# Performance work log

Measured on AMD Instinct MI355X. Metric: run time of the kernel, lower is better.

## Reference

```python
import jax, jax.numpy as jnp
import numpy as np

EPS = 1e-12  # torch F.normalize clamp_min eps
NUM_HEADS = 4


def setup_inputs() -> dict:
    key = jax.random.key(0)
    ks = jax.random.split(key, 6)
    B, N, C = 8, 8192, 256
    x1 = jax.random.normal(ks[0], (B, N, C), dtype=jnp.float32)
    x2 = jax.random.normal(ks[1], (B, N, C), dtype=jnp.float32)
    s = 1.0 / np.sqrt(C)
    Wq = jax.random.normal(ks[2], (C, C), dtype=jnp.float32) * s
    Wk = jax.random.normal(ks[3], (C, C), dtype=jnp.float32) * s
    Wv = jax.random.normal(ks[4], (C, C), dtype=jnp.float32) * s
    Wo = jax.random.normal(ks[5], (C, C), dtype=jnp.float32) * s
    bo = jnp.zeros((C,), dtype=jnp.float32)
    temperature = jnp.ones((NUM_HEADS, 1, 1), dtype=jnp.float32)
    return {"x1": x1, "x2": x2, "Wq": Wq, "Wk": Wk, "Wv": Wv,
            "Wo": Wo, "bo": bo, "temperature": temperature}


def reference(x1, x2, Wq, Wk, Wv, Wo, bo, temperature):
    B, N, C = x1.shape
    H = NUM_HEADS
    d = C // H
    # Linear projections (torch Linear: y = x W^T), then [B,H,d,N] layout
    q = (x1 @ Wq.T).reshape(B, N, H, d).transpose(0, 2, 3, 1)  # [B,H,d,N]
    k = (x2 @ Wk.T).reshape(B, N, H, d).transpose(0, 2, 3, 1)  # [B,H,d,N]
    v = (x2 @ Wv.T).reshape(B, N, H, d).transpose(0, 2, 3, 1)  # [B,H,d,N]
    # L2-normalize along the token axis (dim=-1)
    qn = q / jnp.maximum(jnp.linalg.norm(q, axis=-1, keepdims=True), EPS)
    kn = k / jnp.maximum(jnp.linalg.norm(k, axis=-1, keepdims=True), EPS)
    # Channel-wise cross-covariance attention: [B,H,d,d]
    attn = jnp.einsum('bhdn,bhen->bhde', qn, kn) * temperature
    attn = jax.nn.softmax(attn, axis=-1)
    # (dropout is identity in eval mode)
    x_cross = jnp.einsum('bhde,bhen->bhdn', attn, v)  # [B,H,d,N]
    x_cross = x_cross.transpose(0, 3, 1, 2).reshape(B, N, C)  # [B,N,C]
    return x_cross @ Wo.T + bo
```

## Files before the change

### kernel.cpp

```cpp
#include <hip/hip_runtime.h>
#include <hip/hip_bf16.h>

#define BDIM 8
#define NTOK 8192
#define CDIM 256
#define HEADS 4
#define DHEAD 64
#define MROWS (BDIM * NTOK)
#define NSLAB 16

typedef unsigned short ushort_t;
typedef short bf16x8 __attribute__((ext_vector_type(8)));
typedef float f32x4 __attribute__((ext_vector_type(4)));
typedef unsigned short u16x8 __attribute__((ext_vector_type(8)));
typedef unsigned short u16x4 __attribute__((ext_vector_type(4)));

__device__ inline ushort_t f2bf(float f) {
    __hip_bfloat16 h = __float2bfloat16(f);
    return *reinterpret_cast<ushort_t*>(&h);
}

__device__ inline u16x8 pack8(float4 a, float4 b) {
    u16x8 o;
    o[0] = f2bf(a.x); o[1] = f2bf(a.y); o[2] = f2bf(a.z); o[3] = f2bf(a.w);
    o[4] = f2bf(b.x); o[5] = f2bf(b.y); o[6] = f2bf(b.z); o[7] = f2bf(b.w);
    return o;
}

__global__ __launch_bounds__(256) void zero_kernel(float* __restrict__ p, int n) {
    int i = blockIdx.x * 256 + threadIdx.x;
    if (i < n) p[i] = 0.0f;
}

__global__ __launch_bounds__(256) void proj_mfma(
    const float* __restrict__ x1, const float* __restrict__ x2,
    const float* __restrict__ Wq, const float* __restrict__ Wk,
    const float* __restrict__ Wv,
    ushort_t* __restrict__ qp, ushort_t* __restrict__ kp, ushort_t* __restrict__ vp,
    float* __restrict__ ssq, float* __restrict__ ssk)
{
    const float* A; const float* W; ushort_t* outp; float* ss;
    if (blockIdx.z == 0)      { A = x1; W = Wq; outp = qp; ss = ssq; }
    else if (blockIdx.z == 1) { A = x2; W = Wk; outp = kp; ss = ssk; }
    else                      { A = x2; W = Wv; outp = vp; ss = nullptr; }

    __shared__ ushort_t Asl[2][4096];
    __shared__ ushort_t Bsl[2][4096];
    __shared__ float colss[128];

    const int t = threadIdx.x;
    const int lane = t & 63, w = t >> 6;
    const int l16 = lane & 15, quad = lane >> 4;
    const int m0 = blockIdx.x * 128, c0 = blockIdx.y * 128;
    const int wm = (w >> 1) * 64, wn = (w & 1) * 64;

    const int srow = t >> 1;
    const int skh  = t & 1;

    const float* Ap = A + (size_t)(m0 + srow) * CDIM + skh * 16;
    const float* Wp = W + (size_t)(c0 + srow) * CDIM + skh * 16;

    float4 ga[4], gb[4];
#pragma unroll
    for (int i = 0; i < 4; ++i) {
        ga[i] = *(const float4*)(Ap + i * 4);
        gb[i] = *(const float4*)(Wp + i * 4);
    }

    f32x4 acc[4][4] = {};

#pragma unroll 2
    for (int it = 0; it < 8; ++it) {
        ushort_t* As = Asl[it & 1];
        ushort_t* Bs = Bsl[it & 1];
        *(u16x8*)&As[(skh * 2 + 0) * 1024 + srow * 8] = pack8(ga[0], ga[1]);
        *(u16x8*)&As[(skh * 2 + 1) * 1024 + srow * 8] = pack8(ga[2], ga[3]);
        *(u16x8*)&Bs[(skh * 2 + 0) * 1024 + srow * 8] = pack8(gb[0], gb[1]);
        *(u16x8*)&Bs[(skh * 2 + 1) * 1024 + srow * 8] = pack8(gb[2], gb[3]);
        if (it < 7) {
            int ko = (it + 1) * 32;
#pragma unroll
            for (int i = 0; i < 4; ++i) {
                ga[i] = *(const float4*)(Ap + ko + i * 4);
                gb[i] = *(const float4*)(Wp + ko + i * 4);
            }
        }
        asm volatile("s_waitcnt lgkmcnt(0)" ::: "memory");
        __builtin_amdgcn_s_barrier();
        bf16x8 aF[4], bF[4];
#pragma unroll
        for (int i = 0; i < 4; ++i)
            aF[i] = *(const bf16x8*)&As[quad * 1024 + (wm + i * 16 + l16) * 8];
#pragma unroll
        for (int j = 0; j < 4; ++j)
            bF[j] = *(const bf16x8*)&Bs[quad * 1024 + (wn + j * 16 + l16) * 8];
#pragma unroll
        for (int i = 0; i < 4; ++i)
#pragma unroll
            for (int j = 0; j < 4; ++j)
                acc[i][j] = __builtin_amdgcn_mfma_f32_16x16x32_bf16(aF[i], bF[j], acc[i][j], 0, 0, 0);
    }

#pragma unroll
    for (int i = 0; i < 4; ++i) {
#pragma unroll
        for (int j = 0; j < 4; ++j) {
            int col = c0 + wn + j * 16 + l16;
#pragma unroll
            for (int reg = 0; reg < 4; ++reg) {
                int row = m0 + wm + i * 16 + quad * 4 + reg;
                outp[(size_t)row * CDIM + col] = f2bf(acc[i][j][reg]);
            }
        }
    }

    if (ss) {
        __syncthreads();
        if (t < 128) colss[t] = 0.0f;
        __syncthreads();
#pragma unroll
        for (int j = 0; j < 4; ++j) {
            float s = 0.0f;
#pragma unroll
            for (int i = 0; i < 4; ++i)
#pragma unroll
                for (int reg = 0; reg < 4; ++reg)
                    s += acc[i][j][reg] * acc[i][j][reg];
            atomicAdd(&colss[wn + j * 16 + l16], s);
        }
        __syncthreads();
        if (t < 128) {
            int b = m0 >> 13;
            atomicAdd(&ss[b * CDIM + c0 + t], colss[t]);
        }
    }
}

__global__ __launch_bounds__(256) void gram_mfma(
    const ushort_t* __restrict__ qp, const ushort_t* __restrict__ kp,
    float* __restrict__ Gpart)
{
    constexpr int NS = 144;
    __shared__ ushort_t qs[64 * NS];
    __shared__ ushort_t ks2[64 * NS];
    __shared__ float gsum[4096];

    const int t = threadIdx.x;
    const int lane = t & 63, w = t >> 6;
    const int l16 = lane & 15, quad = lane >> 4;
    const int slab = blockIdx.x, h = blockIdx.y, b = blockIdx.z;
    const size_t base = (size_t)b * NTOK * CDIM + h * DHEAD;

    const int cg  = t >> 5;
    const int ng4 = t & 31;

    for (int i = t; i < 4096; i += 256) gsum[i] = 0.0f;

    f32x4 acc[4][4] = {};

    u16x8 qv[2][4], kv[2][4];
#pragma unroll
    for (int i = 0; i < 4; ++i) {
        size_t g = base + (size_t)(slab * 512 + ng4 * 4 + i) * CDIM + cg * 8;
        qv[0][i] = *(const u16x8*)&qp[g];
        kv[0][i] = *(const u16x8*)&kp[g];
    }

#pragma unroll
    for (int cch = 0; cch < 4; ++cch) {
        const int p = cch & 1;
        __syncthreads();
#pragma unroll
        for (int j = 0; j < 8; ++j) {
            u16x4 wq, wk;
            wq[0] = qv[p][0][j]; wq[1] = qv[p][1][j]; wq[2] = qv[p][2][j]; wq[3] = qv[p][3][j];
            wk[0] = kv[p][0][j]; wk[1] = kv[p][1][j]; wk[2] = kv[p][2][j]; wk[3] = kv[p][3][j];
            *(u16x4*)&qs[(cg * 8 + j) * NS + ng4 * 4] = wq;
            *(u16x4*)&ks2[(cg * 8 + j) * NS + ng4 * 4] = wk;
        }
        if (cch < 3) {
#pragma unroll
            for (int i = 0; i < 4; ++i) {
                size_t g = base + (size_t)(slab * 512 + (cch + 1) * 128 + ng4 * 4 + i) * CDIM + cg * 8;
                qv[p ^ 1][i] = *(const u16x8*)&qp[g];
                kv[p ^ 1][i] = *(const u16x8*)&kp[g];
            }
        }
        __syncthreads();
        bf16x8 aF[4], bF[4];
#pragma unroll
        for (int i = 0; i < 4; ++i)
            aF[i] = *(const bf16x8*)&qs[(i * 16 + l16) * NS + w * 32 + quad * 8];
#pragma unroll
        for (int j = 0; j < 4; ++j)
            bF[j] = *(const bf16x8*)&ks2[(j * 16 + l16) * NS + w * 32 + quad * 8];
#pragma unroll
        for (int i = 0; i < 4; ++i)
#pragma unroll
            for (int j = 0; j < 4; ++j)
                acc[i][j] = __builtin_amdgcn_mfma_f32_16x16x32_bf16(aF[i], bF[j], acc[i][j], 0, 0, 0);
    }

    __syncthreads();
#pragma unroll
    for (int i = 0; i < 4; ++i)
#pragma unroll
        for (int j = 0; j < 4; ++j)
#pragma unroll
            for (int reg = 0; reg < 4; ++reg)
                atomicAdd(&gsum[(i * 16 + quad * 4 + reg) * 64 + j * 16 + l16], acc[i][j][reg]);
    __syncthreads();

    float* Gp = Gpart + ((size_t)slab * BDIM * HEADS + b * HEADS + h) * 4096;
    for (int i = t; i < 4096; i += 256) Gp[i] = gsum[i];
}

__global__ __launch_bounds__(256) void softmax_weff(
    const float* __restrict__ Gpart, const float* __restrict__ ssq,
    const float* __restrict__ ssk, const float* __restrict__ temp,
    const float* __restrict__ Wo, ushort_t* __restrict__ Weffb)
{
    const int h = blockIdx.x, b = blockIdx.y;
    const int t = threadIdx.x;
    __shared__ float at[64][65];
    __shared__ float nk[64];

    if (t < 64) nk[t] = fmaxf(sqrtf(ssk[b * CDIM + h * DHEAD + t]), 1e-12f);
    __syncthreads();

    {
        const int row = t >> 2, part = t & 3;
        const size_t sstride = (size_t)BDIM * HEADS * 4096;
        const float* Gbase = Gpart + (size_t)(b * HEADS + h) * 4096 + row * 64 + part * 16;
        const float tmp = temp[h];
        const float nq = fmaxf(sqrtf(ssq[b * CDIM + h * DHEAD + row]), 1e-12f);

        float sum[16];
#pragma unroll
        for (int j = 0; j < 16; ++j) sum[j] = 0.0f;
#pragma unroll
        for (int s = 0; s < NSLAB; ++s) {
            const float4* gp = (const float4*)(Gbase + (size_t)s * sstride);
#pragma unroll
            for (int q4 = 0; q4 < 4; ++q4) {
                float4 v = gp[q4];
                sum[q4 * 4 + 0] += v.x; sum[q4 * 4 + 1] += v.y;
                sum[q4 * 4 + 2] += v.z; sum[q4 * 4 + 3] += v.w;
            }
        }

        float vals[16];
        float mx = -1e30f;
#pragma unroll
        for (int j = 0; j < 16; ++j) {
            int e = part * 16 + j;
            float v = sum[j] / (nq * nk[e]) * tmp;
            vals[j] = v;
            mx = fmaxf(mx, v);
        }
        mx = fmaxf(mx, __shfl_xor(mx, 1));
        mx = fmaxf(mx, __shfl_xor(mx, 2));
        float s = 0.0f;
#pragma unroll
        for (int j = 0; j < 16; ++j) {
            float ev = __expf(vals[j] - mx);
            vals[j] = ev;
            s += ev;
        }
        s += __shfl_xor(s, 1);
        s += __shfl_xor(s, 2);
        float inv = 1.0f / s;
#pragma unroll
        for (int j = 0; j < 16; ++j)
            at[row][part * 16 + j] = vals[j] * inv;
    }
    __syncthreads();

    const int c = t;
    float wo[64];
#pragma unroll
    for (int d2 = 0; d2 < 64; ++d2) wo[d2] = Wo[(size_t)c * CDIM + h * DHEAD + d2];

    ushort_t* Wb = Weffb + (size_t)b * CDIM * CDIM + (size_t)c * CDIM + h * DHEAD;
#pragma unroll 4
    for (int e = 0; e < 64; ++e) {
        float s = 0.0f;
#pragma unroll
        for (int d2 = 0; d2 < 64; ++d2) s += wo[d2] * at[d2][e];
        Wb[e] = f2bf(s);
    }
}

__global__ __launch_bounds__(256) void out_mfma(
    const ushort_t* __restrict__ vp, const ushort_t* __restrict__ Weffb,
    const float* __restrict__ bo, float* __restrict__ out)
{
    __shared__ ushort_t Asl[2][4096];
    __shared__ ushort_t Bsl[2][4096];

    const int t = threadIdx.x;
    const int lane = t & 63, w = t >> 6;
    const int l16 = lane & 15, quad = lane >> 4;
    const int m0 = blockIdx.x * 128, c0 = blockIdx.y * 128;
    const int wm = (w >> 1) * 64, wn = (w & 1) * 64;

    const int srow = t >> 1;
    const int skh  = t & 1;

    const ushort_t* Ap = vp + (size_t)(m0 + srow) * CDIM + skh * 16;
    const ushort_t* Bp = Weffb + (size_t)(m0 >> 13) * CDIM * CDIM
                       + (size_t)(c0 + srow) * CDIM + skh * 16;

    u16x8 ga0 = *(const u16x8*)Ap,       ga1 = *(const u16x8*)(Ap + 8);
    u16x8 gb0 = *(const u16x8*)Bp,       gb1 = *(const u16x8*)(Bp + 8);

    f32x4 acc[4][4] = {};

#pragma unroll 2
    for (int it = 0; it < 8; ++it) {
        ushort_t* As = Asl[it & 1];
        ushort_t* Bs = Bsl[it & 1];
        *(u16x8*)&As[(skh * 2 + 0) * 1024 + srow * 8] = ga0;
        *(u16x8*)&As[(skh * 2 + 1) * 1024 + srow * 8] = ga1;
        *(u16x8*)&Bs[(skh * 2 + 0) * 1024 + srow * 8] = gb0;
        *(u16x8*)&Bs[(skh * 2 + 1) * 1024 + srow * 8] = gb1;
        if (it < 7) {
            int ko = (it + 1) * 32;
            ga0 = *(const u16x8*)(Ap + ko);
            ga1 = *(const u16x8*)(Ap + ko + 8);
            gb0 = *(const u16x8*)(Bp + ko);
            gb1 = *(const u16x8*)(Bp + ko + 8);
        }
        asm volatile("s_waitcnt lgkmcnt(0)" ::: "memory");
        __builtin_amdgcn_s_barrier();
        bf16x8 aF[4], bF[4];
#pragma unroll
        for (int i = 0; i < 4; ++i)
            aF[i] = *(const bf16x8*)&As[quad * 1024 + (wm + i * 16 + l16) * 8];
#pragma unroll
        for (int j = 0; j < 4; ++j)
            bF[j] = *(const bf16x8*)&Bs[quad * 1024 + (wn + j * 16 + l16) * 8];
#pragma unroll
        for (int i = 0; i < 4; ++i)
#pragma unroll
            for (int j = 0; j < 4; ++j)
                acc[i][j] = __builtin_amdgcn_mfma_f32_16x16x32_bf16(aF[i], bF[j], acc[i][j], 0, 0, 0);
    }

#pragma unroll
    for (int i = 0; i < 4; ++i) {
#pragma unroll
        for (int j = 0; j < 4; ++j) {
            int col = c0 + wn + j * 16 + l16;
            float bias = bo[col];
#pragma unroll
            for (int reg = 0; reg < 4; ++reg) {
                int row = m0 + wm + i * 16 + quad * 4 + reg;
                out[(size_t)row * CDIM + col] = acc[i][j][reg] + bias;
            }
        }
    }
}

extern "C" void kernel_launch(void* const* d_in, const int* in_sizes, int n_in,
                              void* d_out, int out_size, void* d_ws, size_t ws_size,
                              hipStream_t stream) {
    const float* x1   = (const float*)d_in[0];
    const float* x2   = (const float*)d_in[1];
    const float* Wq   = (const float*)d_in[2];
    const float* Wk   = (const float*)d_in[3];
    const float* Wv   = (const float*)d_in[4];
    const float* Wo   = (const float*)d_in[5];
    const float* bo   = (const float*)d_in[6];
    const float* temp = (const float*)d_in[7];
    float* out = (float*)d_out;

    char* ws = (char*)d_ws;
    const size_t SZP = (size_t)MROWS * CDIM * sizeof(ushort_t);
    ushort_t* qp   = (ushort_t*)(ws);
    ushort_t* kp   = (ushort_t*)(ws + SZP);
    ushort_t* vp   = (ushort_t*)(ws + 2 * SZP);
    float*    ssq  = (float*)(ws + 3 * SZP);
    float*    ssk  = (float*)(ws + 3 * SZP + 8192);
    float*    Gpart= (float*)(ws + 3 * SZP + 16384);
    ushort_t* Weffb= (ushort_t*)(ws + 3 * SZP + 16384 + (size_t)NSLAB * BDIM * HEADS * 4096 * 4);

    zero_kernel<<<dim3((4096 + 255) / 256), dim3(256), 0, stream>>>(ssq, 4096);

    proj_mfma<<<dim3(MROWS / 128, CDIM / 128, 3), dim3(256), 0, stream>>>(
        x1, x2, Wq, Wk, Wv, qp, kp, vp, ssq, ssk);

    gram_mfma<<<dim3(NSLAB, HEADS, BDIM), dim3(256), 0, stream>>>(qp, kp, Gpart);

    softmax_weff<<<dim3(HEADS, BDIM), dim3(256), 0, stream>>>(Gpart, ssq, ssk, temp, Wo, Weffb);

    out_mfma<<<dim3(MROWS / 128, CDIM / 128), dim3(256), 0, stream>>>(vp, Weffb, bo, out);
}
```

Before: 351.6 us.

## Stream projection and output GEMMs without LDS using pre-converted bf16 weights

Adds a prep kernel that converts Wq/Wk/Wv to bf16 once and zeroes the sum-of-squares buffers, which replaces the zero kernel. The projection and output GEMMs are rewritten so each block covers 64 rows by all 256 columns. A rows feed straight into MFMA fragments from registers, and weight fragments are read directly from global memory, relying on L2 for reuse. This removes the LDS staging, barriers, and the repeated re-reading and re-conversion of A across column tiles. Column sums of squares use shuffles and one atomic per column per block. The risk is heavy reliance on uncoalesced global weight loads and higher register pressure.

```diff
diff --git a/kernel.cpp b/kernel.cpp
--- a/kernel.cpp
+++ b/kernel.cpp
@@ -27,112 +27,93 @@
     return o;
 }
 
-__global__ __launch_bounds__(256) void zero_kernel(float* __restrict__ p, int n) {
-    int i = blockIdx.x * 256 + threadIdx.x;
-    if (i < n) p[i] = 0.0f;
-}
-
-__global__ __launch_bounds__(256) void proj_mfma(
+__device__ inline bf16x8 as_bf(u16x8 v) { return *(bf16x8*)&v; }
+
+__global__ __launch_bounds__(256) void prep_kernel(
+    const float* __restrict__ Wq, const float* __restrict__ Wk,
+    const float* __restrict__ Wv, ushort_t* __restrict__ wb,
+    float* __restrict__ ss)
+{
+    const int bid = blockIdx.x;
+    if (bid < 96) {
+        int idx = (bid * 256 + threadIdx.x) * 8;
+        const float* src = (idx < 65536) ? Wq : (idx < 131072) ? Wk : Wv;
+        int off = idx & 65535;
+        float4 a = *(const float4*)(src + off);
+        float4 b = *(const float4*)(src + off + 4);
+        *(u16x8*)(wb + idx) = pack8(a, b);
+    } else {
+        int i = (bid - 96) * 256 + threadIdx.x;
+        if (i < 4096) ss[i] = 0.0f;
+    }
+}
+
+__global__ __launch_bounds__(256) void proj_stream(
     const float* __restrict__ x1, const float* __restrict__ x2,
-    const float* __restrict__ Wq, const float* __restrict__ Wk,
-    const float* __restrict__ Wv,
+    const ushort_t* __restrict__ wb,
     ushort_t* __restrict__ qp, ushort_t* __restrict__ kp, ushort_t* __restrict__ vp,
     float* __restrict__ ssq, float* __restrict__ ssk)
 {
-    const float* A; const float* W; ushort_t* outp; float* ss;
-    if (blockIdx.z == 0)      { A = x1; W = Wq; outp = qp; ss = ssq; }
-    else if (blockIdx.z == 1) { A = x2; W = Wk; outp = kp; ss = ssk; }
-    else                      { A = x2; W = Wv; outp = vp; ss = nullptr; }
-
-    __shared__ ushort_t Asl[2][4096];
-    __shared__ ushort_t Bsl[2][4096];
-    __shared__ float colss[128];
+    __shared__ float colw[4][256];
+
+    const float* A; const ushort_t* W; ushort_t* outp; float* ss;
+    if (blockIdx.y == 0)      { A = x1; W = wb;          outp = qp; ss = ssq; }
+    else if (blockIdx.y == 1) { A = x2; W = wb + 65536;  outp = kp; ss = ssk; }
+    else                      { A = x2; W = wb + 131072; outp = vp; ss = nullptr; }
 
     const int t = threadIdx.x;
     const int lane = t & 63, w = t >> 6;
     const int l16 = lane & 15, quad = lane >> 4;
-    const int m0 = blockIdx.x * 128, c0 = blockIdx.y * 128;
-    const int wm = (w >> 1) * 64, wn = (w & 1) * 64;
-
-    const int srow = t >> 1;
-    const int skh  = t & 1;
-
-    const float* Ap = A + (size_t)(m0 + srow) * CDIM + skh * 16;
-    const float* Wp = W + (size_t)(c0 + srow) * CDIM + skh * 16;
-
-    float4 ga[4], gb[4];
-#pragma unroll
-    for (int i = 0; i < 4; ++i) {
-        ga[i] = *(const float4*)(Ap + i * 4);
-        gb[i] = *(const float4*)(Wp + i * 4);
-    }
-
-    f32x4 acc[4][4] = {};
-
-#pragma unroll 2
-    for (int it = 0; it < 8; ++it) {
-        ushort_t* As = Asl[it & 1];
-        ushort_t* Bs = Bsl[it & 1];
-        *(u16x8*)&As[(skh * 2 + 0) * 1024 + srow * 8] = pack8(ga[0], ga[1]);
-        *(u16x8*)&As[(skh * 2 + 1) * 1024 + srow * 8] = pack8(ga[2], ga[3]);
-        *(u16x8*)&Bs[(skh * 2 + 0) * 1024 + srow * 8] = pack8(gb[0], gb[1]);
-        *(u16x8*)&Bs[(skh * 2 + 1) * 1024 + srow * 8] = pack8(gb[2], gb[3]);
-        if (it < 7) {
-            int ko = (it + 1) * 32;
-#pragma unroll
-            for (int i = 0; i < 4; ++i) {
-                ga[i] = *(const float4*)(Ap + ko + i * 4);
-                gb[i] = *(const float4*)(Wp + ko + i * 4);
-            }
-        }
-        asm volatile("s_waitcnt lgkmcnt(0)" ::: "memory");
-        __builtin_amdgcn_s_barrier();
-        bf16x8 aF[4], bF[4];
-#pragma unroll
-        for (int i = 0; i < 4; ++i)
-            aF[i] = *(const bf16x8*)&As[quad * 1024 + (wm + i * 16 + l16) * 8];
-#pragma unroll
-        for (int j = 0; j < 4; ++j)
-            bF[j] = *(const bf16x8*)&Bs[quad * 1024 + (wn + j * 16 + l16) * 8];
-#pragma unroll
-        for (int i = 0; i < 4; ++i)
-#pragma unroll
-            for (int j = 0; j < 4; ++j)
-                acc[i][j] = __builtin_amdgcn_mfma_f32_16x16x32_bf16(aF[i], bF[j], acc[i][j], 0, 0, 0);
-    }
-
-#pragma unroll
-    for (int i = 0; i < 4; ++i) {
-#pragma unroll
-        for (int j = 0; j < 4; ++j) {
-            int col = c0 + wn + j * 16 + l16;
-#pragma unroll
-            for (int reg = 0; reg < 4; ++reg) {
-                int row = m0 + wm + i * 16 + quad * 4 + reg;
-                outp[(size_t)row * CDIM + col] = f2bf(acc[i][j][reg]);
-            }
+    const int row0 = blockIdx.x * 64 + w * 16;
+
+    const float*    Ap = A + (size_t)(row0 + l16) * CDIM + quad * 8;
+    const ushort_t* Bp = W + (size_t)l16 * CDIM + quad * 8;
+
+    f32x4 acc[16] = {};
+
+    float4 a0[2], a1[2];
+    a0[0] = *(const float4*)(Ap);       a1[0] = *(const float4*)(Ap + 4);
+    a0[1] = *(const float4*)(Ap + 32);  a1[1] = *(const float4*)(Ap + 36);
+
+#pragma unroll
+    for (int kk = 0; kk < 8; ++kk) {
+        const int p = kk & 1;
+        u16x8 at = pack8(a0[p], a1[p]);
+        bf16x8 aF = as_bf(at);
+        if (kk < 6) {
+            a0[p] = *(const float4*)(Ap + (kk + 2) * 32);
+            a1[p] = *(const float4*)(Ap + (kk + 2) * 32 + 4);
+        }
+#pragma unroll
+        for (int j = 0; j < 16; ++j) {
+            bf16x8 bF = *(const bf16x8*)(Bp + j * 16 * CDIM + kk * 32);
+            acc[j] = __builtin_amdgcn_mfma_f32_16x16x32_bf16(aF, bF, acc[j], 0, 0, 0);
+        }
+    }
+
+#pragma unroll
+    for (int j = 0; j < 16; ++j) {
+        int col = j * 16 + l16;
+#pragma unroll
+        for (int reg = 0; reg < 4; ++reg) {
+            int row = row0 + quad * 4 + reg;
+            outp[(size_t)row * CDIM + col] = f2bf(acc[j][reg]);
         }
     }
 
     if (ss) {
+#pragma unroll
+        for (int j = 0; j < 16; ++j) {
+            float s = acc[j][0] * acc[j][0] + acc[j][1] * acc[j][1]
+                    + acc[j][2] * acc[j][2] + acc[j][3] * acc[j][3];
+            s += __shfl_xor(s, 16);
+            s += __shfl_xor(s, 32);
+            if (lane < 16) colw[w][j * 16 + l16] = s;
+        }
         __syncthreads();
-        if (t < 128) colss[t] = 0.0f;
-        __syncthreads();
-#pragma unroll
-        for (int j = 0; j < 4; ++j) {
-            float s = 0.0f;
-#pragma unroll
-            for (int i = 0; i < 4; ++i)
-#pragma unroll
-                for (int reg = 0; reg < 4; ++reg)
-                    s += acc[i][j][reg] * acc[i][j][reg];
-            atomicAdd(&colss[wn + j * 16 + l16], s);
-        }
-        __syncthreads();
-        if (t < 128) {
-            int b = m0 >> 13;
-            atomicAdd(&ss[b * CDIM + c0 + t], colss[t]);
-        }
+        float tot = colw[0][t] + colw[1][t] + colw[2][t] + colw[3][t];
+        int b = (blockIdx.x * 64) >> 13;
+        atomicAdd(&ss[b * CDIM + t], tot);
     }
 }
 
@@ -291,73 +272,46 @@
     }
 }
 
-__global__ __launch_bounds__(256) void out_mfma(
+__global__ __launch_bounds__(256) void out_stream(
     const ushort_t* __restrict__ vp, const ushort_t* __restrict__ Weffb,
     const float* __restrict__ bo, float* __restrict__ out)
 {
-    __shared__ ushort_t Asl[2][4096];
-    __shared__ ushort_t Bsl[2][4096];
-
     const int t = threadIdx.x;
     const int lane = t & 63, w = t >> 6;
     const int l16 = lane & 15, quad = lane >> 4;
-    const int m0 = blockIdx.x * 128, c0 = blockIdx.y * 128;
-    const int wm = (w >> 1) * 64, wn = (w & 1) * 64;
-
-    const int srow = t >> 1;
-    const int skh  = t & 1;
-
-    const ushort_t* Ap = vp + (size_t)(m0 + srow) * CDIM + skh * 16;
-    const ushort_t* Bp = Weffb + (size_t)(m0 >> 13) * CDIM * CDIM
-                       + (size_t)(c0 + srow) * CDIM + skh * 16;
-
-    u16x8 ga0 = *(const u16x8*)Ap,       ga1 = *(const u16x8*)(Ap + 8);
-    u16x8 gb0 = *(const u16x8*)Bp,       gb1 = *(const u16x8*)(Bp + 8);
-
-    f32x4 acc[4][4] = {};
-
-#pragma unroll 2
-    for (int it = 0; it < 8; ++it) {
-        ushort_t* As = Asl[it & 1];
-        ushort_t* Bs = Bsl[it & 1];
-        *(u16x8*)&As[(skh * 2 + 0) * 1024 + srow * 8] = ga0;
-        *(u16x8*)&As[(skh * 2 + 1) * 1024 + srow * 8] = ga1;
-        *(u16x8*)&Bs[(skh * 2 + 0) * 1024 + srow * 8] = gb0;
-        *(u16x8*)&Bs[(skh * 2 + 1) * 1024 + srow * 8] = gb1;
-        if (it < 7) {
-            int ko = (it + 1) * 32;
-            ga0 = *(const u16x8*)(Ap + ko);
-            ga1 = *(const u16x8*)(Ap + ko + 8);
-            gb0 = *(const u16x8*)(Bp + ko);
-            gb1 = *(const u16x8*)(Bp + ko + 8);
-        }
-        asm volatile("s_waitcnt lgkmcnt(0)" ::: "memory");
-        __builtin_amdgcn_s_barrier();
-        bf16x8 aF[4], bF[4];
-#pragma unroll
-        for (int i = 0; i < 4; ++i)
-            aF[i] = *(const bf16x8*)&As[quad * 1024 + (wm + i * 16 + l16) * 8];
-#pragma unroll
-        for (int j = 0; j < 4; ++j)
-            bF[j] = *(const bf16x8*)&Bs[quad * 1024 + (wn + j * 16 + l16) * 8];
-#pragma unroll
-        for (int i = 0; i < 4; ++i)
-#pragma unroll
-            for (int j = 0; j < 4; ++j)
-                acc[i][j] = __builtin_amdgcn_mfma_f32_16x16x32_bf16(aF[i], bF[j], acc[i][j], 0, 0, 0);
-    }
-
-#pragma unroll
-    for (int i = 0; i < 4; ++i) {
-#pragma unroll
-        for (int j = 0; j < 4; ++j) {
-            int col = c0 + wn + j * 16 + l16;
-            float bias = bo[col];
-#pragma unroll
-            for (int reg = 0; reg < 4; ++reg) {
-                int row = m0 + wm + i * 16 + quad * 4 + reg;
-                out[(size_t)row * CDIM + col] = acc[i][j][reg] + bias;
-            }
+    const int row0 = blockIdx.x * 64 + w * 16;
+    const int b = (blockIdx.x * 64) >> 13;
+
+    const ushort_t* Ap = vp + (size_t)(row0 + l16) * CDIM + quad * 8;
+    const ushort_t* Bp = Weffb + (size_t)b * CDIM * CDIM + (size_t)l16 * CDIM + quad * 8;
+
+    f32x4 acc[16] = {};
+
+    u16x8 av[2];
+    av[0] = *(const u16x8*)(Ap);
+    av[1] = *(const u16x8*)(Ap + 32);
+
+#pragma unroll
+    for (int kk = 0; kk < 8; ++kk) {
+        const int p = kk & 1;
+        u16x8 at = av[p];
+        bf16x8 aF = as_bf(at);
+        if (kk < 6) av[p] = *(const u16x8*)(Ap + (kk + 2) * 32);
+#pragma unroll
+        for (int j = 0; j < 16; ++j) {
+            bf16x8 bF = *(const bf16x8*)(Bp + j * 16 * CDIM + kk * 32);
+            acc[j] = __builtin_amdgcn_mfma_f32_16x16x32_bf16(aF, bF, acc[j], 0, 0, 0);
+        }
+    }
+
+#pragma unroll
+    for (int j = 0; j < 16; ++j) {
+        int col = j * 16 + l16;
+        float bias = bo[col];
+#pragma unroll
+        for (int reg = 0; reg < 4; ++reg) {
+            int row = row0 + quad * 4 + reg;
+            out[(size_t)row * CDIM + col] = acc[j][reg] + bias;
         }
     }
 }
@@ -383,16 +337,17 @@
     float*    ssq  = (float*)(ws + 3 * SZP);
     float*    ssk  = (float*)(ws + 3 * SZP + 8192);
     float*    Gpart= (float*)(ws + 3 * SZP + 16384);
-    ushort_t* Weffb= (ushort_t*)(ws + 3 * SZP + 16384 + (size_t)NSLAB * BDIM * HEADS * 4096 * 4);
-
-    zero_kernel<<<dim3((4096 + 255) / 256), dim3(256), 0, stream>>>(ssq, 4096);
-
-    proj_mfma<<<dim3(MROWS / 128, CDIM / 128, 3), dim3(256), 0, stream>>>(
-        x1, x2, Wq, Wk, Wv, qp, kp, vp, ssq, ssk);
+    ushort_t* Weffb= (ushort_t*)(ws + 3 * SZP + 16384 + 8388608);
+    ushort_t* wb   = (ushort_t*)(ws + 3 * SZP + 16384 + 8388608 + 1048576);
+
+    prep_kernel<<<dim3(112), dim3(256), 0, stream>>>(Wq, Wk, Wv, wb, ssq);
+
+    proj_stream<<<dim3(MROWS / 64, 3), dim3(256), 0, stream>>>(
+        x1, x2, wb, qp, kp, vp, ssq, ssk);
 
     gram_mfma<<<dim3(NSLAB, HEADS, BDIM), dim3(256), 0, stream>>>(qp, kp, Gpart);
 
     softmax_weff<<<dim3(HEADS, BDIM), dim3(256), 0, stream>>>(Gpart, ssq, ssk, temp, Wo, Weffb);
 
-    out_mfma<<<dim3(MROWS / 128, CDIM / 128), dim3(256), 0, stream>>>(vp, Weffb, bo, out);
-}
+    out_stream<<<dim3(MROWS / 64), dim3(256), 0, stream>>>(vp, Weffb, bo, out);
+}
```

Result: slower. 525.0 us (+49.3%).

## Fold Wv into per-batch effective weight and skip V projection

Applied to the files above, without the earlier changes.

Drops the V projection from the projection kernel and instead folds Wv into the per-batch effective output matrix (Weff·Wv) with a small MFMA kernel. The final GEMM then reads x2 in fp32 directly, converting to bf16 on the fly, instead of reading a bf16 V buffer. This removes a full M×C×C GEMM and the write and read of the V intermediate. The cost is one extra small kernel, twice the fp32 input bytes read in the final GEMM, and an extra bf16 rounding of the combined weight.

```diff
diff --git a/kernel.cpp b/kernel.cpp
--- a/kernel.cpp
+++ b/kernel.cpp
@@ -35,14 +35,12 @@
 __global__ __launch_bounds__(256) void proj_mfma(
     const float* __restrict__ x1, const float* __restrict__ x2,
     const float* __restrict__ Wq, const float* __restrict__ Wk,
-    const float* __restrict__ Wv,
-    ushort_t* __restrict__ qp, ushort_t* __restrict__ kp, ushort_t* __restrict__ vp,
+    ushort_t* __restrict__ qp, ushort_t* __restrict__ kp,
     float* __restrict__ ssq, float* __restrict__ ssk)
 {
     const float* A; const float* W; ushort_t* outp; float* ss;
-    if (blockIdx.z == 0)      { A = x1; W = Wq; outp = qp; ss = ssq; }
-    else if (blockIdx.z == 1) { A = x2; W = Wk; outp = kp; ss = ssk; }
-    else                      { A = x2; W = Wv; outp = vp; ss = nullptr; }
+    if (blockIdx.z == 0) { A = x1; W = Wq; outp = qp; ss = ssq; }
+    else                 { A = x2; W = Wk; outp = kp; ss = ssk; }
 
     __shared__ ushort_t Asl[2][4096];
     __shared__ ushort_t Bsl[2][4096];
@@ -114,25 +112,23 @@
         }
     }
 
-    if (ss) {
-        __syncthreads();
-        if (t < 128) colss[t] = 0.0f;
-        __syncthreads();
-#pragma unroll
-        for (int j = 0; j < 4; ++j) {
-            float s = 0.0f;
-#pragma unroll
-            for (int i = 0; i < 4; ++i)
-#pragma unroll
-                for (int reg = 0; reg < 4; ++reg)
-                    s += acc[i][j][reg] * acc[i][j][reg];
-            atomicAdd(&colss[wn + j * 16 + l16], s);
-        }
-        __syncthreads();
-        if (t < 128) {
-            int b = m0 >> 13;
-            atomicAdd(&ss[b * CDIM + c0 + t], colss[t]);
-        }
+    __syncthreads();
+    if (t < 128) colss[t] = 0.0f;
+    __syncthreads();
+#pragma unroll
+    for (int j = 0; j < 4; ++j) {
+        float s = 0.0f;
+#pragma unroll
+        for (int i = 0; i < 4; ++i)
+#pragma unroll
+            for (int reg = 0; reg < 4; ++reg)
+                s += acc[i][j][reg] * acc[i][j][reg];
+        atomicAdd(&colss[wn + j * 16 + l16], s);
+    }
+    __syncthreads();
+    if (t < 128) {
+        int b = m0 >> 13;
+        atomicAdd(&ss[b * CDIM + c0 + t], colss[t]);
     }
 }
 
@@ -291,8 +287,65 @@
     }
 }
 
-__global__ __launch_bounds__(256) void out_mfma(
-    const ushort_t* __restrict__ vp, const ushort_t* __restrict__ Weffb,
+__global__ __launch_bounds__(256) void w2_kernel(
+    const ushort_t* __restrict__ Weffb, const float* __restrict__ Wv,
+    ushort_t* __restrict__ W2b)
+{
+    __shared__ ushort_t wvt[256 * 264];
+
+    const int t = threadIdx.x;
+    const int lane = t & 63, w = t >> 6;
+    const int l16 = lane & 15, quad = lane >> 4;
+    const int c0 = blockIdx.x * 64;
+    const int b  = blockIdx.y;
+
+#pragma unroll 4
+    for (int s = 0; s < 64; ++s) {
+        int e  = s * 4 + (t >> 6);
+        int k4 = (t & 63) * 4;
+        float4 v = *(const float4*)(Wv + (size_t)e * CDIM + k4);
+        wvt[(k4 + 0) * 264 + e] = f2bf(v.x);
+        wvt[(k4 + 1) * 264 + e] = f2bf(v.y);
+        wvt[(k4 + 2) * 264 + e] = f2bf(v.z);
+        wvt[(k4 + 3) * 264 + e] = f2bf(v.w);
+    }
+    __syncthreads();
+
+    const ushort_t* Ab = Weffb + (size_t)b * CDIM * CDIM;
+    f32x4 acc[4][4] = {};
+
+#pragma unroll
+    for (int kk = 0; kk < 8; ++kk) {
+        bf16x8 aF[4], bF[4];
+#pragma unroll
+        for (int i = 0; i < 4; ++i)
+            aF[i] = *(const bf16x8*)&Ab[(size_t)(c0 + i * 16 + l16) * CDIM + kk * 32 + quad * 8];
+#pragma unroll
+        for (int j = 0; j < 4; ++j)
+            bF[j] = *(const bf16x8*)&wvt[(w * 64 + j * 16 + l16) * 264 + kk * 32 + quad * 8];
+#pragma unroll
+        for (int i = 0; i < 4; ++i)
+#pragma unroll
+            for (int j = 0; j < 4; ++j)
+                acc[i][j] = __builtin_amdgcn_mfma_f32_16x16x32_bf16(aF[i], bF[j], acc[i][j], 0, 0, 0);
+    }
+
+    ushort_t* Wp = W2b + (size_t)b * CDIM * CDIM;
+#pragma unroll
+    for (int i = 0; i < 4; ++i)
+#pragma unroll
+        for (int j = 0; j < 4; ++j) {
+            int k = w * 64 + j * 16 + l16;
+#pragma unroll
+            for (int reg = 0; reg < 4; ++reg) {
+                int c = c0 + i * 16 + quad * 4 + reg;
+                Wp[(size_t)c * CDIM + k] = f2bf(acc[i][j][reg]);
+            }
+        }
+}
+
+__global__ __launch_bounds__(256) void out_x2(
+    const float* __restrict__ x2, const ushort_t* __restrict__ W2b,
     const float* __restrict__ bo, float* __restrict__ out)
 {
     __shared__ ushort_t Asl[2][4096];
@@ -307,12 +360,14 @@
     const int srow = t >> 1;
     const int skh  = t & 1;
 
-    const ushort_t* Ap = vp + (size_t)(m0 + srow) * CDIM + skh * 16;
-    const ushort_t* Bp = Weffb + (size_t)(m0 >> 13) * CDIM * CDIM
+    const float*    Ap = x2 + (size_t)(m0 + srow) * CDIM + skh * 16;
+    const ushort_t* Bp = W2b + (size_t)(m0 >> 13) * CDIM * CDIM
                        + (size_t)(c0 + srow) * CDIM + skh * 16;
 
-    u16x8 ga0 = *(const u16x8*)Ap,       ga1 = *(const u16x8*)(Ap + 8);
-    u16x8 gb0 = *(const u16x8*)Bp,       gb1 = *(const u16x8*)(Bp + 8);
+    float4 ga[4];
+#pragma unroll
+    for (int i = 0; i < 4; ++i) ga[i] = *(const float4*)(Ap + i * 4);
+    u16x8 gb0 = *(const u16x8*)Bp, gb1 = *(const u16x8*)(Bp + 8);
 
     f32x4 acc[4][4] = {};
 
@@ -320,14 +375,14 @@
     for (int it = 0; it < 8; ++it) {
         ushort_t* As = Asl[it & 1];
         ushort_t* Bs = Bsl[it & 1];
-        *(u16x8*)&As[(skh * 2 + 0) * 1024 + srow * 8] = ga0;
-        *(u16x8*)&As[(skh * 2 + 1) * 1024 + srow * 8] = ga1;
+        *(u16x8*)&As[(skh * 2 + 0) * 1024 + srow * 8] = pack8(ga[0], ga[1]);
+        *(u16x8*)&As[(skh * 2 + 1) * 1024 + srow * 8] = pack8(ga[2], ga[3]);
         *(u16x8*)&Bs[(skh * 2 + 0) * 1024 + srow * 8] = gb0;
         *(u16x8*)&Bs[(skh * 2 + 1) * 1024 + srow * 8] = gb1;
         if (it < 7) {
             int ko = (it + 1) * 32;
-            ga0 = *(const u16x8*)(Ap + ko);
-            ga1 = *(const u16x8*)(Ap + ko + 8);
+#pragma unroll
+            for (int i = 0; i < 4; ++i) ga[i] = *(const float4*)(Ap + ko + i * 4);
             gb0 = *(const u16x8*)(Bp + ko);
             gb1 = *(const u16x8*)(Bp + ko + 8);
         }
@@ -379,20 +434,22 @@
     const size_t SZP = (size_t)MROWS * CDIM * sizeof(ushort_t);
     ushort_t* qp   = (ushort_t*)(ws);
     ushort_t* kp   = (ushort_t*)(ws + SZP);
-    ushort_t* vp   = (ushort_t*)(ws + 2 * SZP);
-    float*    ssq  = (float*)(ws + 3 * SZP);
-    float*    ssk  = (float*)(ws + 3 * SZP + 8192);
-    float*    Gpart= (float*)(ws + 3 * SZP + 16384);
-    ushort_t* Weffb= (ushort_t*)(ws + 3 * SZP + 16384 + (size_t)NSLAB * BDIM * HEADS * 4096 * 4);
+    float*    ssq  = (float*)(ws + 2 * SZP);
+    float*    ssk  = (float*)(ws + 2 * SZP + 8192);
+    float*    Gpart= (float*)(ws + 2 * SZP + 16384);
+    ushort_t* Weffb= (ushort_t*)(ws + 2 * SZP + 16384 + 8388608);
+    ushort_t* W2b  = (ushort_t*)(ws + 2 * SZP + 16384 + 8388608 + 1048576);
 
     zero_kernel<<<dim3((4096 + 255) / 256), dim3(256), 0, stream>>>(ssq, 4096);
 
-    proj_mfma<<<dim3(MROWS / 128, CDIM / 128, 3), dim3(256), 0, stream>>>(
-        x1, x2, Wq, Wk, Wv, qp, kp, vp, ssq, ssk);
+    proj_mfma<<<dim3(MROWS / 128, CDIM / 128, 2), dim3(256), 0, stream>>>(
+        x1, x2, Wq, Wk, qp, kp, ssq, ssk);
 
     gram_mfma<<<dim3(NSLAB, HEADS, BDIM), dim3(256), 0, stream>>>(qp, kp, Gpart);
 
     softmax_weff<<<dim3(HEADS, BDIM), dim3(256), 0, stream>>>(Gpart, ssq, ssk, temp, Wo, Weffb);
 
-    out_mfma<<<dim3(MROWS / 128, CDIM / 128), dim3(256), 0, stream>>>(vp, Weffb, bo, out);
-}
+    w2_kernel<<<dim3(4, BDIM), dim3(256), 0, stream>>>(Weffb, Wv, W2b);
+
+    out_x2<<<dim3(MROWS / 128, CDIM / 128), dim3(256), 0, stream>>>(x2, W2b, bo, out);
+}
```

Result: no change. 355.8 us (+1.2%).
